# Optimization experiments

Measured on AMD Instinct MI355X. Metric: run time of the kernel, lower is better.

The kernel has to match this reference:

```python
import jax, jax.numpy as jnp
import numpy as np

N_NODES = 100000
N_EDGES = 1600000
D_IN = 64
D_OUT = 64
NEG_SLOPE = 0.2


def setup_inputs() -> dict:
    key = jax.random.key(0)
    ks = jax.random.split(key, 10)
    x = jax.random.normal(ks[0], (N_NODES, D_IN), dtype=jnp.float32)
    edge_index = jax.random.randint(ks[1], (2, N_EDGES), 0, N_NODES, dtype=jnp.int64)
    # glorot-ish scales
    s_lin = 1.0 / np.sqrt(D_IN)
    W_lin = jax.random.normal(ks[2], (D_IN, D_OUT), dtype=jnp.float32) * s_lin
    att_src = jax.random.normal(ks[3], (D_OUT,), dtype=jnp.float32) * s_lin
    att_dst = jax.random.normal(ks[4], (D_OUT,), dtype=jnp.float32) * s_lin
    bias = jnp.zeros((D_OUT,), dtype=jnp.float32)
    W1 = jax.random.normal(ks[5], (D_IN, D_OUT // 2), dtype=jnp.float32) * s_lin
    b1 = jnp.zeros((D_OUT // 2,), dtype=jnp.float32)
    W2 = jax.random.normal(ks[6], (D_OUT // 2, 1), dtype=jnp.float32) * (1.0 / np.sqrt(D_OUT // 2))
    b2 = jnp.zeros((1,), dtype=jnp.float32)
    return {"x": x, "edge_index": edge_index, "W_lin": W_lin, "att_src": att_src,
            "att_dst": att_dst, "bias": bias, "W1": W1, "b1": b1, "W2": W2, "b2": b2}


def reference(x, edge_index, W_lin, att_src, att_dst, bias, W1, b1, W2, b2):
    N = x.shape[0]
    h = x @ W_lin  # [N, D_OUT]
    # peak detector applied to projected features (module requires in==out)
    peak = jax.nn.sigmoid(jax.nn.gelu(h @ W1 + b1, approximate=False) @ W2 + b2)  # [N,1]
    row, col = edge_index[0], edge_index[1]
    # (cat(src,dst) * att).sum(-1) == (h@att_src)[row] + (h@att_dst)[col]
    a_s = h @ att_src  # [N]
    a_d = h @ att_dst  # [N]
    alpha = a_s[row] + a_d[col]  # [E]
    alpha = jnp.where(alpha >= 0, alpha, NEG_SLOPE * alpha)  # leaky_relu
    # segment softmax keyed on row
    m = jax.ops.segment_max(alpha, row, num_segments=N)  # [N]
    e = jnp.exp(alpha - m[row])
    s = jax.ops.segment_sum(e, row, num_segments=N)  # [N]
    alpha = e / s[row]
    # scatter-add weighted source messages back to row (dropout=identity in eval)
    out = jax.ops.segment_sum(h[row] * alpha[:, None], row, num_segments=N)  # [N, D_OUT]
    out = out * (1.0 + peak) + bias
    return out
```

## Files before the change

### kernel.cpp

```cpp
#include <hip/hip_runtime.h>
#include <math.h>

#define D 64
#define DH 32

typedef __attribute__((ext_vector_type(8))) short bf16x8;
typedef __attribute__((ext_vector_type(4))) float f32x4;

static __device__ __forceinline__ unsigned short f2b(float f) {
    unsigned int u = __builtin_bit_cast(unsigned int, f);
    u += 0x7FFFu + ((u >> 16) & 1u);
    return (unsigned short)(u >> 16);
}
static __device__ __forceinline__ unsigned int pack_b2(float a, float b) {
    return (unsigned int)f2b(a) | ((unsigned int)f2b(b) << 16);
}
static __device__ __forceinline__ float gelu_fast(float v) {
    const float ax = fabsf(v) * 0.70710678118654752f;
    const float t  = __builtin_amdgcn_rcpf(fmaf(0.3275911f, ax, 1.0f));
    float poly = fmaf(1.061405429f, t, -1.453152027f);
    poly = fmaf(poly, t, 1.421413741f);
    poly = fmaf(poly, t, -0.284496736f);
    poly = fmaf(poly, t, 0.254829592f);
    poly *= t;
    float er = fmaf(-poly, __expf(-ax * ax), 1.0f);
    er = copysignf(er, v);
    return 0.5f * v * (1.0f + er);
}

__global__ void edge_flag_kernel(const int* __restrict__ row,
                                 unsigned char* __restrict__ flag, int E) {
    const int base = (blockIdx.x * blockDim.x + threadIdx.x) * 8;
    if (base + 7 < E) {
        const int4 a = *(const int4*)(row + base);
        const int4 b = *(const int4*)(row + base + 4);
        flag[a.x] = 1; flag[a.y] = 1; flag[a.z] = 1; flag[a.w] = 1;
        flag[b.x] = 1; flag[b.y] = 1; flag[b.z] = 1; flag[b.w] = 1;
    } else if (base < E) {
        for (int j = base; j < E; ++j) flag[row[j]] = 1;
    }
}

__global__ __launch_bounds__(256) void gat_mfma6(
    const float* __restrict__ x, const unsigned char* __restrict__ flag,
    const float* __restrict__ Wlin, const float* __restrict__ bias,
    const float* __restrict__ W1, const float* __restrict__ b1,
    const float* __restrict__ W2, const float* __restrict__ b2,
    float* __restrict__ out, int N, int ntiles)
{
    __shared__ unsigned short sH[4][16][72];

    const int tid  = threadIdx.x;
    const int wv   = tid >> 6;
    const int lane = tid & 63;
    const int q    = lane >> 4;
    const int m    = lane & 15;

    bf16x8 aw[4][2], aw1[2][2];
#pragma unroll
    for (int nt = 0; nt < 4; ++nt)
#pragma unroll
        for (int ks = 0; ks < 2; ++ks) {
            bf16x8 a;
#pragma unroll
            for (int j = 0; j < 8; ++j)
                a[j] = (short)f2b(Wlin[(32 * ks + 8 * q + j) * D + 16 * nt + m]);
            aw[nt][ks] = a;
        }
#pragma unroll
    for (int nt = 0; nt < 2; ++nt)
#pragma unroll
        for (int ks = 0; ks < 2; ++ks) {
            bf16x8 a;
#pragma unroll
            for (int j = 0; j < 8; ++j)
                a[j] = (short)f2b(W1[(32 * ks + 8 * q + j) * DH + 16 * nt + m]);
            aw1[nt][ks] = a;
        }
    f32x4 b1v0, b1v1, w2v0, w2v1;
    f32x4 biasv[4];
#pragma unroll
    for (int r = 0; r < 4; ++r) {
        b1v0[r] = b1[4 * q + r];
        b1v1[r] = b1[16 + 4 * q + r];
        w2v0[r] = W2[4 * q + r];
        w2v1[r] = W2[16 + 4 * q + r];
#pragma unroll
        for (int nt = 0; nt < 4; ++nt)
            biasv[nt][r] = bias[16 * nt + 4 * q + r];
    }
    const float b2s = b2[0];

    int t = blockIdx.x;
    if (t >= ntiles) return;

    float4 cu0, cu1, cu2, cu3; unsigned char cfl;
    {
        int g = t * 64 + wv * 16 + m; if (g > N - 1) g = N - 1;
        const float* px = x + (size_t)g * D + 8 * q;
        cu0 = *(const float4*)(px);      cu1 = *(const float4*)(px + 4);
        cu2 = *(const float4*)(px + 32); cu3 = *(const float4*)(px + 36);
        cfl = flag[g];
    }

    while (true) {
        const int tn = t + gridDim.x;
        const bool more = tn < ntiles;
        float4 nu0, nu1, nu2, nu3; unsigned char nfl = 0;
        if (more) {
            int g = tn * 64 + wv * 16 + m; if (g > N - 1) g = N - 1;
            const float* px = x + (size_t)g * D + 8 * q;
            nu0 = *(const float4*)(px);      nu1 = *(const float4*)(px + 4);
            nu2 = *(const float4*)(px + 32); nu3 = *(const float4*)(px + 36);
            nfl = flag[g];
        }

        uint4 pk0, pk1;
        pk0.x = pack_b2(cu0.x, cu0.y); pk0.y = pack_b2(cu0.z, cu0.w);
        pk0.z = pack_b2(cu1.x, cu1.y); pk0.w = pack_b2(cu1.z, cu1.w);
        pk1.x = pack_b2(cu2.x, cu2.y); pk1.y = pack_b2(cu2.z, cu2.w);
        pk1.z = pack_b2(cu3.x, cu3.y); pk1.w = pack_b2(cu3.z, cu3.w);
        const bf16x8 bx0 = __builtin_bit_cast(bf16x8, pk0);
        const bf16x8 bx1 = __builtin_bit_cast(bf16x8, pk1);

        f32x4 accH[4];
#pragma unroll
        for (int nt = 0; nt < 4; ++nt) accH[nt] = (f32x4){0.f, 0.f, 0.f, 0.f};
#pragma unroll
        for (int nt = 0; nt < 4; ++nt)
            accH[nt] = __builtin_amdgcn_mfma_f32_16x16x32_bf16(aw[nt][0], bx0, accH[nt], 0, 0, 0);
#pragma unroll
        for (int nt = 0; nt < 4; ++nt)
            accH[nt] = __builtin_amdgcn_mfma_f32_16x16x32_bf16(aw[nt][1], bx1, accH[nt], 0, 0, 0);

        asm volatile("" ::: "memory");
#pragma unroll
        for (int nt = 0; nt < 4; ++nt) {
            uint2 pk;
            pk.x = pack_b2(accH[nt][0], accH[nt][1]);
            pk.y = pack_b2(accH[nt][2], accH[nt][3]);
            *(uint2*)&sH[wv][m][16 * nt + 4 * q] = pk;
        }
        asm volatile("" ::: "memory");
        const bf16x8 a20 = *(const bf16x8*)&sH[wv][m][8 * q];
        const bf16x8 a21 = *(const bf16x8*)&sH[wv][m][32 + 8 * q];

        f32x4 acc20 = b1v0, acc21 = b1v1;
        acc20 = __builtin_amdgcn_mfma_f32_16x16x32_bf16(aw1[0][0], a20, acc20, 0, 0, 0);
        acc20 = __builtin_amdgcn_mfma_f32_16x16x32_bf16(aw1[0][1], a21, acc20, 0, 0, 0);
        acc21 = __builtin_amdgcn_mfma_f32_16x16x32_bf16(aw1[1][0], a20, acc21, 0, 0, 0);
        acc21 = __builtin_amdgcn_mfma_f32_16x16x32_bf16(aw1[1][1], a21, acc21, 0, 0, 0);

        float pp = 0.f;
#pragma unroll
        for (int r = 0; r < 4; ++r) {
            pp = fmaf(gelu_fast(acc20[r]), w2v0[r], pp);
            pp = fmaf(gelu_fast(acc21[r]), w2v1[r], pp);
        }
        pp += __shfl_xor(pp, 16);
        pp += __shfl_xor(pp, 32);
        const float sg = __builtin_amdgcn_rcpf(1.f + __expf(-(pp + b2s)));
        const float scale = (cfl != 0) ? (1.f + sg) : 0.f;

        const int g = t * 64 + wv * 16 + m;
        if (g < N) {
            float* po = out + (size_t)g * D + 4 * q;
#pragma unroll
            for (int nt = 0; nt < 4; ++nt) {
                f32x4 o;
#pragma unroll
                for (int r = 0; r < 4; ++r)
                    o[r] = fmaf(accH[nt][r], scale, biasv[nt][r]);
                *(f32x4*)(po + 16 * nt) = o;
            }
        }

        if (!more) break;
        cu0 = nu0; cu1 = nu1; cu2 = nu2; cu3 = nu3; cfl = nfl;
        t = tn;
    }
}

extern "C" void kernel_launch(void* const* d_in, const int* in_sizes, int n_in,
                              void* d_out, int out_size, void* d_ws, size_t ws_size,
                              hipStream_t stream) {
    const float* x    = (const float*)d_in[0];
    const int*   eidx = (const int*)d_in[1];
    const float* Wlin = (const float*)d_in[2];
    const float* bias = (const float*)d_in[5];
    const float* W1   = (const float*)d_in[6];
    const float* b1   = (const float*)d_in[7];
    const float* W2   = (const float*)d_in[8];
    const float* b2   = (const float*)d_in[9];
    float* out = (float*)d_out;

    const int N = in_sizes[0] / D;
    const int E = in_sizes[1] / 2;

    unsigned char* flag = (unsigned char*)d_ws;

    const int ntiles  = (N + 63) / 64;
    const int nblocks = (ntiles < 512) ? ntiles : 512;

    hipMemsetAsync(flag, 0, (size_t)N, stream);
    edge_flag_kernel<<<(E / 8 + 255) / 256, 256, 0, stream>>>(eidx, flag, E);
    gat_mfma6<<<nblocks, 256, 0, stream>>>(x, flag, Wlin, bias, W1, b1, W2, b2,
                                           out, N, ntiles);
}
```

Baseline: 32.43 us.

## Precompute Wlin@W1 product to drop LDS round-trip for peak MLP

A new tiny kernel computes W1p = Wlin·W1 (in bf16 MFMA) once per call, so the peak-detector first layer can be applied directly to x instead of to h. This removes the per-tile bf16 packing of h, the shared-memory store/load and the dependency between the two MFMA stages. The x-to-bf16 packing also switches to the hardware v_cvt_pk_bf16_f32 instruction. The cost is an extra kernel launch. Rounding changes because the product is formed once and rounded to bf16.

```diff
diff --git a/kernel.cpp b/kernel.cpp
--- a/kernel.cpp
+++ b/kernel.cpp
@@ -14,6 +14,11 @@
 }
 static __device__ __forceinline__ unsigned int pack_b2(float a, float b) {
     return (unsigned int)f2b(a) | ((unsigned int)f2b(b) << 16);
+}
+static __device__ __forceinline__ unsigned int cvtpk(float a, float b) {
+    unsigned int r;
+    asm("v_cvt_pk_bf16_f32 %0, %1, %2" : "=v"(r) : "v"(a), "v"(b));
+    return r;
 }
 static __device__ __forceinline__ float gelu_fast(float v) {
     const float ax = fabsf(v) * 0.70710678118654752f;
@@ -41,22 +46,62 @@
     }
 }
 
-__global__ __launch_bounds__(256) void gat_mfma6(
+__global__ __launch_bounds__(256) void prep_w1p(const float* __restrict__ Wlin,
+                                                const float* __restrict__ W1,
+                                                float* __restrict__ W1p)
+{
+    const int lane = threadIdx.x & 63, w = threadIdx.x >> 6;
+    const int q = lane >> 4, m = lane & 15;
+    const int i = 16 * w + m;
+
+    const float* px = Wlin + i * D + 8 * q;
+    const float4 cu0 = *(const float4*)(px);      const float4 cu1 = *(const float4*)(px + 4);
+    const float4 cu2 = *(const float4*)(px + 32); const float4 cu3 = *(const float4*)(px + 36);
+    uint4 pk0, pk1;
+    pk0.x = pack_b2(cu0.x, cu0.y); pk0.y = pack_b2(cu0.z, cu0.w);
+    pk0.z = pack_b2(cu1.x, cu1.y); pk0.w = pack_b2(cu1.z, cu1.w);
+    pk1.x = pack_b2(cu2.x, cu2.y); pk1.y = pack_b2(cu2.z, cu2.w);
+    pk1.z = pack_b2(cu3.x, cu3.y); pk1.w = pack_b2(cu3.z, cu3.w);
+    const bf16x8 bx0 = __builtin_bit_cast(bf16x8, pk0);
+    const bf16x8 bx1 = __builtin_bit_cast(bf16x8, pk1);
+
+    bf16x8 a1[2][2];
+#pragma unroll
+    for (int nt = 0; nt < 2; ++nt)
+#pragma unroll
+        for (int ks = 0; ks < 2; ++ks) {
+            bf16x8 a;
+#pragma unroll
+            for (int j = 0; j < 8; ++j)
+                a[j] = (short)f2b(W1[(32 * ks + 8 * q + j) * DH + 16 * nt + m]);
+            a1[nt][ks] = a;
+        }
+    f32x4 acc[2];
+    acc[0] = (f32x4){0.f, 0.f, 0.f, 0.f}; acc[1] = acc[0];
+#pragma unroll
+    for (int nt = 0; nt < 2; ++nt) {
+        acc[nt] = __builtin_amdgcn_mfma_f32_16x16x32_bf16(a1[nt][0], bx0, acc[nt], 0, 0, 0);
+        acc[nt] = __builtin_amdgcn_mfma_f32_16x16x32_bf16(a1[nt][1], bx1, acc[nt], 0, 0, 0);
+    }
+#pragma unroll
+    for (int nt = 0; nt < 2; ++nt)
+        *(f32x4*)&W1p[i * DH + 16 * nt + 4 * q] = acc[nt];
+}
+
+__global__ __launch_bounds__(256) void gat_mfma9(
     const float* __restrict__ x, const unsigned char* __restrict__ flag,
     const float* __restrict__ Wlin, const float* __restrict__ bias,
-    const float* __restrict__ W1, const float* __restrict__ b1,
+    const float* __restrict__ W1p_g, const float* __restrict__ b1,
     const float* __restrict__ W2, const float* __restrict__ b2,
     float* __restrict__ out, int N, int ntiles)
 {
-    __shared__ unsigned short sH[4][16][72];
-
     const int tid  = threadIdx.x;
     const int wv   = tid >> 6;
     const int lane = tid & 63;
     const int q    = lane >> 4;
     const int m    = lane & 15;
 
-    bf16x8 aw[4][2], aw1[2][2];
+    bf16x8 aw[4][2], awp[2][2];
 #pragma unroll
     for (int nt = 0; nt < 4; ++nt)
 #pragma unroll
@@ -74,8 +119,8 @@
             bf16x8 a;
 #pragma unroll
             for (int j = 0; j < 8; ++j)
-                a[j] = (short)f2b(W1[(32 * ks + 8 * q + j) * DH + 16 * nt + m]);
-            aw1[nt][ks] = a;
+                a[j] = (short)f2b(W1p_g[(32 * ks + 8 * q + j) * DH + 16 * nt + m]);
+            awp[nt][ks] = a;
         }
     f32x4 b1v0, b1v1, w2v0, w2v1;
     f32x4 biasv[4];
@@ -116,10 +161,10 @@
         }
 
         uint4 pk0, pk1;
-        pk0.x = pack_b2(cu0.x, cu0.y); pk0.y = pack_b2(cu0.z, cu0.w);
-        pk0.z = pack_b2(cu1.x, cu1.y); pk0.w = pack_b2(cu1.z, cu1.w);
-        pk1.x = pack_b2(cu2.x, cu2.y); pk1.y = pack_b2(cu2.z, cu2.w);
-        pk1.z = pack_b2(cu3.x, cu3.y); pk1.w = pack_b2(cu3.z, cu3.w);
+        pk0.x = cvtpk(cu0.x, cu0.y); pk0.y = cvtpk(cu0.z, cu0.w);
+        pk0.z = cvtpk(cu1.x, cu1.y); pk0.w = cvtpk(cu1.z, cu1.w);
+        pk1.x = cvtpk(cu2.x, cu2.y); pk1.y = cvtpk(cu2.z, cu2.w);
+        pk1.z = cvtpk(cu3.x, cu3.y); pk1.w = cvtpk(cu3.z, cu3.w);
         const bf16x8 bx0 = __builtin_bit_cast(bf16x8, pk0);
         const bf16x8 bx1 = __builtin_bit_cast(bf16x8, pk1);
 
@@ -133,23 +178,11 @@
         for (int nt = 0; nt < 4; ++nt)
             accH[nt] = __builtin_amdgcn_mfma_f32_16x16x32_bf16(aw[nt][1], bx1, accH[nt], 0, 0, 0);
 
-        asm volatile("" ::: "memory");
-#pragma unroll
-        for (int nt = 0; nt < 4; ++nt) {
-            uint2 pk;
-            pk.x = pack_b2(accH[nt][0], accH[nt][1]);
-            pk.y = pack_b2(accH[nt][2], accH[nt][3]);
-            *(uint2*)&sH[wv][m][16 * nt + 4 * q] = pk;
-        }
-        asm volatile("" ::: "memory");
-        const bf16x8 a20 = *(const bf16x8*)&sH[wv][m][8 * q];
-        const bf16x8 a21 = *(const bf16x8*)&sH[wv][m][32 + 8 * q];
-
         f32x4 acc20 = b1v0, acc21 = b1v1;
-        acc20 = __builtin_amdgcn_mfma_f32_16x16x32_bf16(aw1[0][0], a20, acc20, 0, 0, 0);
-        acc20 = __builtin_amdgcn_mfma_f32_16x16x32_bf16(aw1[0][1], a21, acc20, 0, 0, 0);
-        acc21 = __builtin_amdgcn_mfma_f32_16x16x32_bf16(aw1[1][0], a20, acc21, 0, 0, 0);
-        acc21 = __builtin_amdgcn_mfma_f32_16x16x32_bf16(aw1[1][1], a21, acc21, 0, 0, 0);
+        acc20 = __builtin_amdgcn_mfma_f32_16x16x32_bf16(awp[0][0], bx0, acc20, 0, 0, 0);
+        acc20 = __builtin_amdgcn_mfma_f32_16x16x32_bf16(awp[0][1], bx1, acc20, 0, 0, 0);
+        acc21 = __builtin_amdgcn_mfma_f32_16x16x32_bf16(awp[1][0], bx0, acc21, 0, 0, 0);
+        acc21 = __builtin_amdgcn_mfma_f32_16x16x32_bf16(awp[1][1], bx1, acc21, 0, 0, 0);
 
         float pp = 0.f;
 #pragma unroll
@@ -197,13 +230,17 @@
     const int N = in_sizes[0] / D;
     const int E = in_sizes[1] / 2;
 
-    unsigned char* flag = (unsigned char*)d_ws;
+    char* ws = (char*)d_ws;
+    unsigned char* flag = (unsigned char*)ws;
+    const size_t off = (((size_t)N) + 255) & ~(size_t)255;
+    float* W1p = (float*)(ws + off);
 
     const int ntiles  = (N + 63) / 64;
     const int nblocks = (ntiles < 512) ? ntiles : 512;
 
-    hipMemsetAsync(flag, 0, (size_t)N, stream);
+    (void)hipMemsetAsync(flag, 0, (size_t)N, stream);
+    prep_w1p<<<1, 256, 0, stream>>>(Wlin, W1, W1p);
     edge_flag_kernel<<<(E / 8 + 255) / 256, 256, 0, stream>>>(eidx, flag, E);
-    gat_mfma6<<<nblocks, 256, 0, stream>>>(x, flag, Wlin, bias, W1, b1, W2, b2,
+    gat_mfma9<<<nblocks, 256, 0, stream>>>(x, flag, Wlin, bias, W1p, b1, W2, b2,
                                            out, N, ntiles);
 }
```

New measurement: 34.53 us. 1.06x slower.
